# Kernel optimization log

Hardware: AMD Instinct MI355X
Metric: run time of the kernel (lower is better)

## Reference

```python
import jax, jax.numpy as jnp
import numpy as np

EPS = 1e-6
N_HEADS = 32
N_KV_HEADS = 8
HEAD_DIM = 64


def _rmsnorm(x, scale):
    xf = x.astype(jnp.float32)
    y = xf * jax.lax.rsqrt(jnp.mean(xf * xf, axis=-1, keepdims=True) + EPS)
    return y.astype(x.dtype) * scale


def _rope(t, cos, sin):
    # t: [B,S,H,D]; cos/sin: [S,D//2] -> broadcast [1,S,1,D//2]
    tr = t.reshape(*t.shape[:-1], HEAD_DIM // 2, 2)
    tre, tim = tr[..., 0], tr[..., 1]
    c = cos[None, :, None, :]
    s = sin[None, :, None, :]
    out_re = tre * c - tim * s
    out_im = tre * s + tim * c
    return jnp.stack([out_re, out_im], axis=-1).reshape(t.shape)


def setup_inputs() -> dict:
    key = jax.random.key(0)
    ks = jax.random.split(key, 8)
    B, S, D = 2, 2048, 2048
    x = jax.random.normal(ks[0], (B, S, D), dtype=jnp.float32)
    # rotary freqs: cos/sin of theta^(-2i/d) * pos, like precompute_freqs_cis
    pos = jnp.arange(S, dtype=jnp.float32)
    inv_freq = 1.0 / (10000.0 ** (jnp.arange(0, HEAD_DIM, 2, dtype=jnp.float32) / HEAD_DIM))
    angles = pos[:, None] * inv_freq[None, :]  # [S, D/2]
    freqs_cos = jnp.cos(angles)
    freqs_sin = jnp.sin(angles)
    std = 0.02
    wq = jax.random.normal(ks[1], (N_HEADS * HEAD_DIM, D), dtype=jnp.float32) * std
    wk = jax.random.normal(ks[2], (N_KV_HEADS * HEAD_DIM, D), dtype=jnp.float32) * std
    wv = jax.random.normal(ks[3], (N_KV_HEADS * HEAD_DIM, D), dtype=jnp.float32) * std
    wo = jax.random.normal(ks[4], (D, N_HEADS * HEAD_DIM), dtype=jnp.float32) * std
    q_scale = jnp.ones((HEAD_DIM,), dtype=jnp.float32)
    k_scale = jnp.ones((HEAD_DIM,), dtype=jnp.float32)
    return {"x": x, "freqs_cos": freqs_cos, "freqs_sin": freqs_sin,
            "wq": wq, "wk": wk, "wv": wv, "wo": wo,
            "q_scale": q_scale, "k_scale": k_scale}


def reference(x, freqs_cos, freqs_sin, wq, wk, wv, wo, q_scale, k_scale):
    B, S, D = x.shape
    n_rep = N_HEADS // N_KV_HEADS
    xq = (x @ wq.T).reshape(B, S, N_HEADS, HEAD_DIM)
    xk = (x @ wk.T).reshape(B, S, N_KV_HEADS, HEAD_DIM)
    xv = (x @ wv.T).reshape(B, S, N_KV_HEADS, HEAD_DIM)
    # per-head QK RMSNorm
    xq = _rmsnorm(xq, q_scale)
    xk = _rmsnorm(xk, k_scale)
    # rotary embedding
    xq = _rope(xq, freqs_cos, freqs_sin)
    xk = _rope(xk, freqs_cos, freqs_sin)
    # GQA repeat_kv
    keys = jnp.repeat(xk, n_rep, axis=2)    # [B,S,H,Dh]
    values = jnp.repeat(xv, n_rep, axis=2)
    # SDPA, causal
    q = xq.transpose(0, 2, 1, 3)  # [B,H,S,Dh]
    k = keys.transpose(0, 2, 1, 3)
    v = values.transpose(0, 2, 1, 3)
    scale = 1.0 / jnp.sqrt(jnp.float32(HEAD_DIM))
    scores = jnp.einsum('bhqd,bhkd->bhqk', q, k) * scale
    causal = jnp.tril(jnp.ones((S, S), dtype=bool))
    scores = jnp.where(causal[None, None], scores, jnp.finfo(scores.dtype).min)
    probs = jax.nn.softmax(scores, axis=-1)
    out = jnp.einsum('bhqk,bhkd->bhqd', probs, v)
    out = out.transpose(0, 2, 1, 3).reshape(B, S, N_HEADS * HEAD_DIM)
    return out @ wo.T
```

## Files before the change

kernel.cpp:

```cpp
#include <hip/hip_runtime.h>
#include <hip/hip_bf16.h>
#include <math.h>

#define S_LEN   2048
#define DMODEL  2048
#define NHEADS  32
#define NKV     8
#define HD      64
#define MTOK    4096
#define KVDIM   512

typedef short s16x8 __attribute__((ext_vector_type(8)));
typedef float f32x4 __attribute__((ext_vector_type(4)));

__device__ __forceinline__ ushort f2bf(float f) {
    union { float f; uint u; } a; a.f = f;
    return (ushort)((a.u + 0x7fffu + ((a.u >> 16) & 1u)) >> 16);
}
__device__ __forceinline__ float bf2f(ushort h) {
    union { uint u; float f; } a; a.u = ((uint)h) << 16; return a.f;
}

__global__ __launch_bounds__(256) void csplit(const float* __restrict__ src,
                                              ushort* __restrict__ dh,
                                              ushort* __restrict__ dl, int n8) {
    const int i = blockIdx.x * 256 + threadIdx.x;
    if (i >= n8) return;
    float4 a = ((const float4*)src)[2 * i];
    float4 b = ((const float4*)src)[2 * i + 1];
    float f[8] = {a.x, a.y, a.z, a.w, b.x, b.y, b.z, b.w};
    s16x8 h, l;
#pragma unroll
    for (int j = 0; j < 8; ++j) {
        ushort hb = f2bf(f[j]);
        h[j] = (short)hb;
        l[j] = (short)f2bf(f[j] - bf2f(hb));
    }
    ((s16x8*)dh)[i] = h;
    ((s16x8*)dl)[i] = l;
}

__global__ __launch_bounds__(256) void gemm_bs(const ushort* __restrict__ Ahg,
                                               const ushort* __restrict__ Alg,
                                               const ushort* __restrict__ Bhg,
                                               const ushort* __restrict__ Blg,
                                               float* __restrict__ C,
                                               int M, int N, int K) {
    __shared__ ushort Ah[128 * 32];
    __shared__ ushort Al[128 * 32];
    __shared__ ushort Bh[128 * 32];
    __shared__ ushort Bl[128 * 32];

    const int tid  = threadIdx.x;
    const int wave = tid >> 6;
    const int lane = tid & 63;
    const int wr   = (wave >> 1) * 64;
    const int wc   = (wave & 1) * 64;
    const int m0   = blockIdx.y * 128;
    const int n0   = blockIdx.x * 128;

    const int srow = tid >> 2;
    const int skq  = (tid & 3) * 8;
    const int soff = srow * 32 + skq;

    const ushort* pAh = Ahg + (size_t)(m0 + srow) * K + skq;
    const ushort* pAl = Alg + (size_t)(m0 + srow) * K + skq;
    const ushort* pBh = Bhg + (size_t)(n0 + srow) * K + skq;
    const ushort* pBl = Blg + (size_t)(n0 + srow) * K + skq;
    const size_t r64 = (size_t)64 * K;

    const int frow = lane & 15;
    const int fk   = (lane >> 4) * 8;

    f32x4 acc[4][4] = {};

    s16x8 rAh0 = *(const s16x8*)(pAh), rAh1 = *(const s16x8*)(pAh + r64);
    s16x8 rAl0 = *(const s16x8*)(pAl), rAl1 = *(const s16x8*)(pAl + r64);
    s16x8 rBh0 = *(const s16x8*)(pBh), rBh1 = *(const s16x8*)(pBh + r64);
    s16x8 rBl0 = *(const s16x8*)(pBl), rBl1 = *(const s16x8*)(pBl + r64);

    for (int k0 = 0; k0 < K; k0 += 32) {
        __syncthreads();
        *(s16x8*)(Ah + soff) = rAh0;  *(s16x8*)(Ah + soff + 64 * 32) = rAh1;
        *(s16x8*)(Al + soff) = rAl0;  *(s16x8*)(Al + soff + 64 * 32) = rAl1;
        *(s16x8*)(Bh + soff) = rBh0;  *(s16x8*)(Bh + soff + 64 * 32) = rBh1;
        *(s16x8*)(Bl + soff) = rBl0;  *(s16x8*)(Bl + soff + 64 * 32) = rBl1;

        if (k0 + 32 < K) {
            rAh0 = *(const s16x8*)(pAh + k0 + 32); rAh1 = *(const s16x8*)(pAh + r64 + k0 + 32);
            rAl0 = *(const s16x8*)(pAl + k0 + 32); rAl1 = *(const s16x8*)(pAl + r64 + k0 + 32);
            rBh0 = *(const s16x8*)(pBh + k0 + 32); rBh1 = *(const s16x8*)(pBh + r64 + k0 + 32);
            rBl0 = *(const s16x8*)(pBl + k0 + 32); rBl1 = *(const s16x8*)(pBl + r64 + k0 + 32);
        }
        __syncthreads();

        s16x8 ah[4], al[4], bh[4], bl[4];
#pragma unroll
        for (int mi = 0; mi < 4; ++mi) {
            int off = (wr + mi * 16 + frow) * 32 + fk;
            ah[mi] = *(const s16x8*)(Ah + off);
            al[mi] = *(const s16x8*)(Al + off);
        }
#pragma unroll
        for (int nj = 0; nj < 4; ++nj) {
            int off = (wc + nj * 16 + frow) * 32 + fk;
            bh[nj] = *(const s16x8*)(Bh + off);
            bl[nj] = *(const s16x8*)(Bl + off);
        }
#pragma unroll
        for (int mi = 0; mi < 4; ++mi)
#pragma unroll
            for (int nj = 0; nj < 4; ++nj) {
                acc[mi][nj] = __builtin_amdgcn_mfma_f32_16x16x32_bf16(ah[mi], bh[nj], acc[mi][nj], 0, 0, 0);
                acc[mi][nj] = __builtin_amdgcn_mfma_f32_16x16x32_bf16(ah[mi], bl[nj], acc[mi][nj], 0, 0, 0);
                acc[mi][nj] = __builtin_amdgcn_mfma_f32_16x16x32_bf16(al[mi], bh[nj], acc[mi][nj], 0, 0, 0);
            }
    }

    const int crow = (lane >> 4) * 4;
    const int ccol = lane & 15;
#pragma unroll
    for (int mi = 0; mi < 4; ++mi)
#pragma unroll
        for (int r = 0; r < 4; ++r) {
            float* cp = C + (size_t)(m0 + wr + mi * 16 + crow + r) * N + n0 + wc + ccol;
#pragma unroll
            for (int nj = 0; nj < 4; ++nj)
                cp[nj * 16] = acc[mi][nj][r];
        }
}

__global__ __launch_bounds__(256) void rmsrope_split(const float* __restrict__ src,
                                                     const float* __restrict__ scale,
                                                     const float* __restrict__ fcos,
                                                     const float* __restrict__ fsin,
                                                     int nheads, int rowstride,
                                                     ushort* __restrict__ dh,
                                                     ushort* __restrict__ dl,
                                                     float prescale) {
    const int wid   = blockIdx.x * 4 + (threadIdx.x >> 6);
    const int lane  = threadIdx.x & 63;
    const int token = wid / nheads;
    const int h     = wid - token * nheads;
    const int s     = token & (S_LEN - 1);

    const size_t idx = (size_t)token * rowstride + h * HD + lane;
    float v = src[idx];

    float ss = v * v;
#pragma unroll
    for (int off = 32; off; off >>= 1) ss += __shfl_xor(ss, off);

    float y = v * (1.0f / sqrtf(ss * (1.0f / 64.0f) + 1e-6f)) * scale[lane];

    const int j = lane >> 1;
    float c  = fcos[s * (HD / 2) + j];
    float sn = fsin[s * (HD / 2) + j];
    float partner = __shfl_xor(y, 1);
    float o = (lane & 1) ? fmaf(partner, sn, y * c)
                         : fmaf(y, c, -partner * sn);
    o *= prescale;

    ushort hb = f2bf(o);
    dh[idx] = hb;
    dl[idx] = f2bf(o - bf2f(hb));
}

__global__ __launch_bounds__(256) void vtrans(const float* __restrict__ xv,
                                              ushort* __restrict__ vh,
                                              ushort* __restrict__ vl) {
    __shared__ float T[64][65];
    const int tid = threadIdx.x;
    const int st  = blockIdx.x;
    const int bk  = blockIdx.y;
    const int b   = bk >> 3, kvh = bk & 7;

    const int r = tid >> 2, cq = (tid & 3) * 16;
    const float* src = xv + (size_t)(b * S_LEN + st * 64 + r) * KVDIM + kvh * HD + cq;
#pragma unroll
    for (int i = 0; i < 4; ++i) {
        float4 f = *(const float4*)(src + 4 * i);
        T[r][cq + 4 * i + 0] = f.x; T[r][cq + 4 * i + 1] = f.y;
        T[r][cq + 4 * i + 2] = f.z; T[r][cq + 4 * i + 3] = f.w;
    }
    __syncthreads();

    const int d = tid >> 2, sq = (tid & 3) * 16;
    s16x8 hv[2], lv[2];
#pragma unroll
    for (int half = 0; half < 2; ++half)
#pragma unroll
        for (int j = 0; j < 8; ++j) {
            float f = T[sq + half * 8 + j][d];
            ushort hb = f2bf(f);
            hv[half][j] = (short)hb;
            lv[half][j] = (short)f2bf(f - bf2f(hb));
        }
    ushort* oh = vh + (size_t)(bk * HD + d) * S_LEN + st * 64 + sq;
    ushort* ol = vl + (size_t)(bk * HD + d) * S_LEN + st * 64 + sq;
    *(s16x8*)(oh) = hv[0]; *(s16x8*)(oh + 8) = hv[1];
    *(s16x8*)(ol) = lv[0]; *(s16x8*)(ol + 8) = lv[1];
}

__global__ __launch_bounds__(256) void flash_attn(const ushort* __restrict__ qh_g,
                                                  const ushort* __restrict__ ql_g,
                                                  const ushort* __restrict__ kh_g,
                                                  const ushort* __restrict__ kl_g,
                                                  const ushort* __restrict__ vh_g,
                                                  const ushort* __restrict__ vl_g,
                                                  float* __restrict__ ao) {
    __shared__ ushort Kh[64 * 72];
    __shared__ ushort Kl[64 * 72];
    __shared__ ushort Vh[64 * 72];
    __shared__ ushort Vl[64 * 72];
    __shared__ ushort Ph[4][32 * 72];
    __shared__ ushort Pl[4][32 * 72];

    const int tid    = threadIdx.x;
    const int w      = tid >> 6;
    const int lanelo = tid & 15;
    const int g      = (tid >> 4) & 3;
    const int bh     = blockIdx.y;
    const int b      = bh >> 5;
    const int h      = bh & 31;
    const int kvh    = h >> 2;

    const int srow = tid >> 2;
    const int sh   = (tid & 3) * 16;

    const ushort* kbh = kh_g + (size_t)(b * S_LEN) * KVDIM + kvh * HD;
    const ushort* kbl = kl_g + (size_t)(b * S_LEN) * KVDIM + kvh * HD;
    const ushort* vbh = vh_g + (size_t)((b * NKV + kvh) * HD) * S_LEN;
    const ushort* vbl = vl_g + (size_t)((b * NKV + kvh) * HD) * S_LEN;

#pragma unroll 1
    for (int sub = 0; sub < 2; ++sub) {
        const int qt  = sub ? (15 - blockIdx.x) : blockIdx.x;
        const int q0  = qt * 128;
        const int nkt = 2 * qt + 2;

        s16x8 qfh[2][2], qfl[2][2];
#pragma unroll
        for (int mi = 0; mi < 2; ++mi) {
            const size_t qoff = (size_t)(b * S_LEN + q0 + 32 * w + 16 * mi + lanelo) * DMODEL
                              + h * HD + 8 * g;
            qfh[mi][0] = *(const s16x8*)(qh_g + qoff);
            qfh[mi][1] = *(const s16x8*)(qh_g + qoff + 32);
            qfl[mi][0] = *(const s16x8*)(ql_g + qoff);
            qfl[mi][1] = *(const s16x8*)(ql_g + qoff + 32);
        }

        s16x8 rkh0, rkh1, rkl0, rkl1, rvh0, rvh1, rvl0, rvl1;
        {
            const size_t ko = (size_t)srow * KVDIM + sh;
            const size_t vo = (size_t)srow * S_LEN + sh;
            rkh0 = *(const s16x8*)(kbh + ko);  rkh1 = *(const s16x8*)(kbh + ko + 8);
            rkl0 = *(const s16x8*)(kbl + ko);  rkl1 = *(const s16x8*)(kbl + ko + 8);
            rvh0 = *(const s16x8*)(vbh + vo);  rvh1 = *(const s16x8*)(vbh + vo + 8);
            rvl0 = *(const s16x8*)(vbl + vo);  rvl1 = *(const s16x8*)(vbl + vo + 8);
        }

        float m_[2][4], l_[2][4];
        f32x4 O[2][4] = {};
#pragma unroll
        for (int mi = 0; mi < 2; ++mi)
#pragma unroll
            for (int r = 0; r < 4; ++r) { m_[mi][r] = -1e30f; l_[mi][r] = 0.0f; }

        for (int kt = 0; kt < nkt; ++kt) {
            __syncthreads();
            const int lo = srow * 72 + sh;
            *(s16x8*)(Kh + lo) = rkh0;  *(s16x8*)(Kh + lo + 8) = rkh1;
            *(s16x8*)(Kl + lo) = rkl0;  *(s16x8*)(Kl + lo + 8) = rkl1;
            *(s16x8*)(Vh + lo) = rvh0;  *(s16x8*)(Vh + lo + 8) = rvh1;
            *(s16x8*)(Vl + lo) = rvl0;  *(s16x8*)(Vl + lo + 8) = rvl1;
            if (kt + 1 < nkt) {
                const size_t ko = (size_t)((kt + 1) * 64 + srow) * KVDIM + sh;
                const size_t vo = (size_t)srow * S_LEN + (kt + 1) * 64 + sh;
                rkh0 = *(const s16x8*)(kbh + ko);  rkh1 = *(const s16x8*)(kbh + ko + 8);
                rkl0 = *(const s16x8*)(kbl + ko);  rkl1 = *(const s16x8*)(kbl + ko + 8);
                rvh0 = *(const s16x8*)(vbh + vo);  rvh1 = *(const s16x8*)(vbh + vo + 8);
                rvl0 = *(const s16x8*)(vbl + vo);  rvl1 = *(const s16x8*)(vbl + vo + 8);
            }
            __syncthreads();

            f32x4 sc[2][4] = {};
#pragma unroll
            for (int n = 0; n < 4; ++n) {
                const int off = (16 * n + lanelo) * 72 + 8 * g;
                s16x8 kh0 = *(const s16x8*)(Kh + off), kh1 = *(const s16x8*)(Kh + off + 32);
                s16x8 kl0 = *(const s16x8*)(Kl + off), kl1 = *(const s16x8*)(Kl + off + 32);
#pragma unroll
                for (int mi = 0; mi < 2; ++mi) {
                    sc[mi][n] = __builtin_amdgcn_mfma_f32_16x16x32_bf16(qfh[mi][0], kh0, sc[mi][n], 0, 0, 0);
                    sc[mi][n] = __builtin_amdgcn_mfma_f32_16x16x32_bf16(qfh[mi][1], kh1, sc[mi][n], 0, 0, 0);
                    sc[mi][n] = __builtin_amdgcn_mfma_f32_16x16x32_bf16(qfh[mi][0], kl0, sc[mi][n], 0, 0, 0);
                    sc[mi][n] = __builtin_amdgcn_mfma_f32_16x16x32_bf16(qfh[mi][1], kl1, sc[mi][n], 0, 0, 0);
                    sc[mi][n] = __builtin_amdgcn_mfma_f32_16x16x32_bf16(qfl[mi][0], kh0, sc[mi][n], 0, 0, 0);
                    sc[mi][n] = __builtin_amdgcn_mfma_f32_16x16x32_bf16(qfl[mi][1], kh1, sc[mi][n], 0, 0, 0);
                }
            }

            if (kt >= 2 * qt) {
#pragma unroll
                for (int mi = 0; mi < 2; ++mi)
#pragma unroll
                    for (int n = 0; n < 4; ++n) {
                        const int key = kt * 64 + 16 * n + lanelo;
                        const int qrow = q0 + 32 * w + 16 * mi + 4 * g;
#pragma unroll
                        for (int r = 0; r < 4; ++r)
                            if (key > qrow + r) sc[mi][n][r] = -1e30f;
                    }
            }

#pragma unroll
            for (int mi = 0; mi < 2; ++mi)
#pragma unroll
                for (int r = 0; r < 4; ++r) {
                    float mx = fmaxf(fmaxf(sc[mi][0][r], sc[mi][1][r]),
                                     fmaxf(sc[mi][2][r], sc[mi][3][r]));
#pragma unroll
                    for (int off = 1; off < 16; off <<= 1) mx = fmaxf(mx, __shfl_xor(mx, off));
                    float mnew = fmaxf(m_[mi][r], mx);
                    float corr = __expf(m_[mi][r] - mnew);
                    float ps = 0.f;
#pragma unroll
                    for (int n = 0; n < 4; ++n) {
                        float p = __expf(sc[mi][n][r] - mnew);
                        ushort phb = f2bf(p);
                        const int po = (16 * mi + 4 * g + r) * 72 + 16 * n + lanelo;
                        Ph[w][po] = phb;
                        Pl[w][po] = f2bf(p - bf2f(phb));
                        ps += p;
                    }
#pragma unroll
                    for (int off = 1; off < 16; off <<= 1) ps += __shfl_xor(ps, off);
                    l_[mi][r] = l_[mi][r] * corr + ps;
                    m_[mi][r] = mnew;
#pragma unroll
                    for (int n = 0; n < 4; ++n) O[mi][n][r] *= corr;
                }

            s16x8 pf[2][4];
#pragma unroll
            for (int mi = 0; mi < 2; ++mi) {
                const int po = (16 * mi + lanelo) * 72 + 8 * g;
                pf[mi][0] = *(const s16x8*)(Ph[w] + po);
                pf[mi][1] = *(const s16x8*)(Ph[w] + po + 32);
                pf[mi][2] = *(const s16x8*)(Pl[w] + po);
                pf[mi][3] = *(const s16x8*)(Pl[w] + po + 32);
            }
#pragma unroll
            for (int n = 0; n < 4; ++n) {
                const int vo = (16 * n + lanelo) * 72 + 8 * g;
                s16x8 vh0 = *(const s16x8*)(Vh + vo), vh1 = *(const s16x8*)(Vh + vo + 32);
                s16x8 vl0 = *(const s16x8*)(Vl + vo), vl1 = *(const s16x8*)(Vl + vo + 32);
#pragma unroll
                for (int mi = 0; mi < 2; ++mi) {
                    O[mi][n] = __builtin_amdgcn_mfma_f32_16x16x32_bf16(pf[mi][0], vh0, O[mi][n], 0, 0, 0);
                    O[mi][n] = __builtin_amdgcn_mfma_f32_16x16x32_bf16(pf[mi][1], vh1, O[mi][n], 0, 0, 0);
                    O[mi][n] = __builtin_amdgcn_mfma_f32_16x16x32_bf16(pf[mi][0], vl0, O[mi][n], 0, 0, 0);
                    O[mi][n] = __builtin_amdgcn_mfma_f32_16x16x32_bf16(pf[mi][1], vl1, O[mi][n], 0, 0, 0);
                    O[mi][n] = __builtin_amdgcn_mfma_f32_16x16x32_bf16(pf[mi][2], vh0, O[mi][n], 0, 0, 0);
                    O[mi][n] = __builtin_amdgcn_mfma_f32_16x16x32_bf16(pf[mi][3], vh1, O[mi][n], 0, 0, 0);
                }
            }
        }

#pragma unroll
        for (int mi = 0; mi < 2; ++mi)
#pragma unroll
            for (int n = 0; n < 4; ++n)
#pragma unroll
                for (int r = 0; r < 4; ++r) {
                    const int q = q0 + 32 * w + 16 * mi + 4 * g + r;
                    ao[(size_t)(b * S_LEN + q) * DMODEL + h * HD + 16 * n + lanelo] =
                        O[mi][n][r] / l_[mi][r];
                }
    }
}

extern "C" void kernel_launch(void* const* d_in, const int* in_sizes, int n_in,
                              void* d_out, int out_size, void* d_ws, size_t ws_size,
                              hipStream_t stream) {
    const float* x  = (const float*)d_in[0];
    const float* fc = (const float*)d_in[1];
    const float* fs = (const float*)d_in[2];
    const float* wq = (const float*)d_in[3];
    const float* wk = (const float*)d_in[4];
    const float* wv = (const float*)d_in[5];
    const float* wo = (const float*)d_in[6];
    const float* qs = (const float*)d_in[7];
    const float* ks = (const float*)d_in[8];
    float* out = (float*)d_out;

    char* p = (char*)d_ws;
    auto take = [&](size_t bytes) { char* r = p; p += bytes; return r; };
    ushort* wqh = (ushort*)take(8388608);   ushort* wql = (ushort*)take(8388608);
    ushort* wkh = (ushort*)take(2097152);   ushort* wkl = (ushort*)take(2097152);
    ushort* wvh = (ushort*)take(2097152);   ushort* wvl = (ushort*)take(2097152);
    ushort* woh = (ushort*)take(8388608);   ushort* wol = (ushort*)take(8388608);
    ushort* xh  = (ushort*)take(16777216);  ushort* xl  = (ushort*)take(16777216);
    float*  xq32 = (float*)take(33554432);
    float*  xk32 = (float*)take(8388608);
    float*  xv32 = (float*)take(8388608);
    ushort* qh  = (ushort*)take(16777216);  ushort* ql  = (ushort*)take(16777216);
    ushort* kh  = (ushort*)take(4194304);   ushort* kl  = (ushort*)take(4194304);
    ushort* vth = (ushort*)take(4194304);   ushort* vtl = (ushort*)take(4194304);
    ushort* aoh = xh;
    ushort* aol = xl;
    float*  ao32 = xq32;

    csplit<<<4096, 256, 0, stream>>>(x,  xh,  xl,  1048576);
    csplit<<<2048, 256, 0, stream>>>(wq, wqh, wql, 524288);
    csplit<<<512,  256, 0, stream>>>(wk, wkh, wkl, 131072);
    csplit<<<512,  256, 0, stream>>>(wv, wvh, wvl, 131072);
    csplit<<<2048, 256, 0, stream>>>(wo, woh, wol, 524288);

    gemm_bs<<<dim3(16, 32), 256, 0, stream>>>(xh, xl, wqh, wql, xq32, MTOK, DMODEL, DMODEL);
    gemm_bs<<<dim3(4,  32), 256, 0, stream>>>(xh, xl, wkh, wkl, xk32, MTOK, KVDIM,  DMODEL);
    gemm_bs<<<dim3(4,  32), 256, 0, stream>>>(xh, xl, wvh, wvl, xv32, MTOK, KVDIM,  DMODEL);

    rmsrope_split<<<MTOK * NHEADS / 4, 256, 0, stream>>>(xq32, qs, fc, fs, NHEADS, DMODEL, qh, ql, 0.125f);
    rmsrope_split<<<MTOK * NKV / 4,    256, 0, stream>>>(xk32, ks, fc, fs, NKV,    KVDIM,  kh, kl, 1.0f);
    vtrans<<<dim3(32, 16), 256, 0, stream>>>(xv32, vth, vtl);

    flash_attn<<<dim3(8, 64), 256, 0, stream>>>(qh, ql, kh, kl, vth, vtl, ao32);

    csplit<<<4096, 256, 0, stream>>>(ao32, aoh, aol, 1048576);
    gemm_bs<<<dim3(16, 32), 256, 0, stream>>>(aoh, aol, woh, wol, out, MTOK, DMODEL, DMODEL);
}
```

Baseline: 694.4 us.

## Use direct global-to-LDS loads, merge K/V GEMMs, fuse output split into attention

The GEMM stops staging tiles through registers and uses global_load_lds to copy 16-byte chunks straight into shared memory. This drops the register prefetch, so loads are no longer overlapped with compute across iterations. The K and V weight matrices are concatenated so a single GEMM produces both projections. The attention kernel now writes the bf16 hi/lo split of its output directly, removing one fp32 round trip and a separate split kernel, and the P split is simplified to truncation instead of rounding.

```diff
diff --git a/kernel.cpp b/kernel.cpp
--- a/kernel.cpp
+++ b/kernel.cpp
@@ -19,6 +19,12 @@
 }
 __device__ __forceinline__ float bf2f(ushort h) {
     union { uint u; float f; } a; a.u = ((uint)h) << 16; return a.f;
+}
+
+__device__ __forceinline__ void gload16(const void* g, void* l) {
+    __builtin_amdgcn_global_load_lds(
+        (const __attribute__((address_space(1))) void*)g,
+        (__attribute__((address_space(3))) void*)l, 16, 0, 0);
 }
 
 __global__ __launch_bounds__(256) void csplit(const float* __restrict__ src,
@@ -61,7 +67,6 @@
 
     const int srow = tid >> 2;
     const int skq  = (tid & 3) * 8;
-    const int soff = srow * 32 + skq;
 
     const ushort* pAh = Ahg + (size_t)(m0 + srow) * K + skq;
     const ushort* pAl = Alg + (size_t)(m0 + srow) * K + skq;
@@ -69,29 +74,22 @@
     const ushort* pBl = Blg + (size_t)(n0 + srow) * K + skq;
     const size_t r64 = (size_t)64 * K;
 
+    ushort* const lA0  = Ah + wave * 512;  ushort* const lA1  = Ah + 64 * 32 + wave * 512;
+    ushort* const lAl0 = Al + wave * 512;  ushort* const lAl1 = Al + 64 * 32 + wave * 512;
+    ushort* const lB0  = Bh + wave * 512;  ushort* const lB1  = Bh + 64 * 32 + wave * 512;
+    ushort* const lBl0 = Bl + wave * 512;  ushort* const lBl1 = Bl + 64 * 32 + wave * 512;
+
     const int frow = lane & 15;
     const int fk   = (lane >> 4) * 8;
 
     f32x4 acc[4][4] = {};
 
-    s16x8 rAh0 = *(const s16x8*)(pAh), rAh1 = *(const s16x8*)(pAh + r64);
-    s16x8 rAl0 = *(const s16x8*)(pAl), rAl1 = *(const s16x8*)(pAl + r64);
-    s16x8 rBh0 = *(const s16x8*)(pBh), rBh1 = *(const s16x8*)(pBh + r64);
-    s16x8 rBl0 = *(const s16x8*)(pBl), rBl1 = *(const s16x8*)(pBl + r64);
-
     for (int k0 = 0; k0 < K; k0 += 32) {
         __syncthreads();
-        *(s16x8*)(Ah + soff) = rAh0;  *(s16x8*)(Ah + soff + 64 * 32) = rAh1;
-        *(s16x8*)(Al + soff) = rAl0;  *(s16x8*)(Al + soff + 64 * 32) = rAl1;
-        *(s16x8*)(Bh + soff) = rBh0;  *(s16x8*)(Bh + soff + 64 * 32) = rBh1;
-        *(s16x8*)(Bl + soff) = rBl0;  *(s16x8*)(Bl + soff + 64 * 32) = rBl1;
-
-        if (k0 + 32 < K) {
-            rAh0 = *(const s16x8*)(pAh + k0 + 32); rAh1 = *(const s16x8*)(pAh + r64 + k0 + 32);
-            rAl0 = *(const s16x8*)(pAl + k0 + 32); rAl1 = *(const s16x8*)(pAl + r64 + k0 + 32);
-            rBh0 = *(const s16x8*)(pBh + k0 + 32); rBh1 = *(const s16x8*)(pBh + r64 + k0 + 32);
-            rBl0 = *(const s16x8*)(pBl + k0 + 32); rBl1 = *(const s16x8*)(pBl + r64 + k0 + 32);
-        }
+        gload16(pAh + k0, lA0);        gload16(pAh + r64 + k0, lA1);
+        gload16(pAl + k0, lAl0);       gload16(pAl + r64 + k0, lAl1);
+        gload16(pBh + k0, lB0);        gload16(pBh + r64 + k0, lB1);
+        gload16(pBl + k0, lBl0);       gload16(pBl + r64 + k0, lBl1);
         __syncthreads();
 
         s16x8 ah[4], al[4], bh[4], bl[4];
@@ -134,7 +132,7 @@
                                                      const float* __restrict__ scale,
                                                      const float* __restrict__ fcos,
                                                      const float* __restrict__ fsin,
-                                                     int nheads, int rowstride,
+                                                     int nheads, int instride, int outstride,
                                                      ushort* __restrict__ dh,
                                                      ushort* __restrict__ dl,
                                                      float prescale) {
@@ -144,8 +142,7 @@
     const int h     = wid - token * nheads;
     const int s     = token & (S_LEN - 1);
 
-    const size_t idx = (size_t)token * rowstride + h * HD + lane;
-    float v = src[idx];
+    float v = src[(size_t)token * instride + h * HD + lane];
 
     float ss = v * v;
 #pragma unroll
@@ -161,12 +158,14 @@
                          : fmaf(y, c, -partner * sn);
     o *= prescale;
 
+    const size_t oidx = (size_t)token * outstride + h * HD + lane;
     ushort hb = f2bf(o);
-    dh[idx] = hb;
-    dl[idx] = f2bf(o - bf2f(hb));
+    dh[oidx] = hb;
+    dl[oidx] = f2bf(o - bf2f(hb));
 }
 
 __global__ __launch_bounds__(256) void vtrans(const float* __restrict__ xv,
+                                              int instride,
                                               ushort* __restrict__ vh,
                                               ushort* __restrict__ vl) {
     __shared__ float T[64][65];
@@ -176,7 +175,7 @@
     const int b   = bk >> 3, kvh = bk & 7;
 
     const int r = tid >> 2, cq = (tid & 3) * 16;
-    const float* src = xv + (size_t)(b * S_LEN + st * 64 + r) * KVDIM + kvh * HD + cq;
+    const float* src = xv + (size_t)(b * S_LEN + st * 64 + r) * instride + kvh * HD + cq;
 #pragma unroll
     for (int i = 0; i < 4; ++i) {
         float4 f = *(const float4*)(src + 4 * i);
@@ -208,7 +207,8 @@
                                                   const ushort* __restrict__ kl_g,
                                                   const ushort* __restrict__ vh_g,
                                                   const ushort* __restrict__ vl_g,
-                                                  float* __restrict__ ao) {
+                                                  ushort* __restrict__ aoh,
+                                                  ushort* __restrict__ aol) {
     __shared__ ushort Kh[64 * 72];
     __shared__ ushort Kl[64 * 72];
     __shared__ ushort Vh[64 * 72];
@@ -232,6 +232,9 @@
     const ushort* kbl = kl_g + (size_t)(b * S_LEN) * KVDIM + kvh * HD;
     const ushort* vbh = vh_g + (size_t)((b * NKV + kvh) * HD) * S_LEN;
     const ushort* vbl = vl_g + (size_t)((b * NKV + kvh) * HD) * S_LEN;
+
+    ushort* const Phw = Ph[w];
+    ushort* const Plw = Pl[w];
 
 #pragma unroll 1
     for (int sub = 0; sub < 2; ++sub) {
@@ -328,10 +331,11 @@
 #pragma unroll
                     for (int n = 0; n < 4; ++n) {
                         float p = __expf(sc[mi][n][r] - mnew);
-                        ushort phb = f2bf(p);
+                        uint pu = __float_as_uint(p);
+                        float plo = p - __uint_as_float(pu & 0xffff0000u);
                         const int po = (16 * mi + 4 * g + r) * 72 + 16 * n + lanelo;
-                        Ph[w][po] = phb;
-                        Pl[w][po] = f2bf(p - bf2f(phb));
+                        Phw[po] = (ushort)(pu >> 16);
+                        Plw[po] = (ushort)(__float_as_uint(plo) >> 16);
                         ps += p;
                     }
 #pragma unroll
@@ -346,10 +350,10 @@
 #pragma unroll
             for (int mi = 0; mi < 2; ++mi) {
                 const int po = (16 * mi + lanelo) * 72 + 8 * g;
-                pf[mi][0] = *(const s16x8*)(Ph[w] + po);
-                pf[mi][1] = *(const s16x8*)(Ph[w] + po + 32);
-                pf[mi][2] = *(const s16x8*)(Pl[w] + po);
-                pf[mi][3] = *(const s16x8*)(Pl[w] + po + 32);
+                pf[mi][0] = *(const s16x8*)(Phw + po);
+                pf[mi][1] = *(const s16x8*)(Phw + po + 32);
+                pf[mi][2] = *(const s16x8*)(Plw + po);
+                pf[mi][3] = *(const s16x8*)(Plw + po + 32);
             }
 #pragma unroll
             for (int n = 0; n < 4; ++n) {
@@ -375,8 +379,11 @@
 #pragma unroll
                 for (int r = 0; r < 4; ++r) {
                     const int q = q0 + 32 * w + 16 * mi + 4 * g + r;
-                    ao[(size_t)(b * S_LEN + q) * DMODEL + h * HD + 16 * n + lanelo] =
-                        O[mi][n][r] / l_[mi][r];
+                    const size_t o = (size_t)(b * S_LEN + q) * DMODEL + h * HD + 16 * n + lanelo;
+                    float v = O[mi][n][r] / l_[mi][r];
+                    ushort hb = f2bf(v);
+                    aoh[o] = hb;
+                    aol[o] = f2bf(v - bf2f(hb));
                 }
     }
 }
@@ -397,37 +404,32 @@
 
     char* p = (char*)d_ws;
     auto take = [&](size_t bytes) { char* r = p; p += bytes; return r; };
-    ushort* wqh = (ushort*)take(8388608);   ushort* wql = (ushort*)take(8388608);
-    ushort* wkh = (ushort*)take(2097152);   ushort* wkl = (ushort*)take(2097152);
-    ushort* wvh = (ushort*)take(2097152);   ushort* wvl = (ushort*)take(2097152);
-    ushort* woh = (ushort*)take(8388608);   ushort* wol = (ushort*)take(8388608);
-    ushort* xh  = (ushort*)take(16777216);  ushort* xl  = (ushort*)take(16777216);
-    float*  xq32 = (float*)take(33554432);
-    float*  xk32 = (float*)take(8388608);
-    float*  xv32 = (float*)take(8388608);
-    ushort* qh  = (ushort*)take(16777216);  ushort* ql  = (ushort*)take(16777216);
-    ushort* kh  = (ushort*)take(4194304);   ushort* kl  = (ushort*)take(4194304);
-    ushort* vth = (ushort*)take(4194304);   ushort* vtl = (ushort*)take(4194304);
+    ushort* wqh  = (ushort*)take(8388608);   ushort* wql  = (ushort*)take(8388608);
+    ushort* wkvh = (ushort*)take(4194304);   ushort* wkvl = (ushort*)take(4194304);
+    ushort* woh  = (ushort*)take(8388608);   ushort* wol  = (ushort*)take(8388608);
+    ushort* xh   = (ushort*)take(16777216);  ushort* xl   = (ushort*)take(16777216);
+    float*  xq32  = (float*)take(33554432);
+    float*  xkv32 = (float*)take(16777216);
+    ushort* qh   = (ushort*)take(16777216);  ushort* ql   = (ushort*)take(16777216);
+    ushort* kh   = (ushort*)take(4194304);   ushort* kl   = (ushort*)take(4194304);
+    ushort* vth  = (ushort*)take(4194304);   ushort* vtl  = (ushort*)take(4194304);
     ushort* aoh = xh;
     ushort* aol = xl;
-    float*  ao32 = xq32;
 
     csplit<<<4096, 256, 0, stream>>>(x,  xh,  xl,  1048576);
     csplit<<<2048, 256, 0, stream>>>(wq, wqh, wql, 524288);
-    csplit<<<512,  256, 0, stream>>>(wk, wkh, wkl, 131072);
-    csplit<<<512,  256, 0, stream>>>(wv, wvh, wvl, 131072);
+    csplit<<<512,  256, 0, stream>>>(wk, wkvh,                wkvl,                131072);
+    csplit<<<512,  256, 0, stream>>>(wv, wkvh + 512 * DMODEL, wkvl + 512 * DMODEL, 131072);
     csplit<<<2048, 256, 0, stream>>>(wo, woh, wol, 524288);
 
-    gemm_bs<<<dim3(16, 32), 256, 0, stream>>>(xh, xl, wqh, wql, xq32, MTOK, DMODEL, DMODEL);
-    gemm_bs<<<dim3(4,  32), 256, 0, stream>>>(xh, xl, wkh, wkl, xk32, MTOK, KVDIM,  DMODEL);
-    gemm_bs<<<dim3(4,  32), 256, 0, stream>>>(xh, xl, wvh, wvl, xv32, MTOK, KVDIM,  DMODEL);
-
-    rmsrope_split<<<MTOK * NHEADS / 4, 256, 0, stream>>>(xq32, qs, fc, fs, NHEADS, DMODEL, qh, ql, 0.125f);
-    rmsrope_split<<<MTOK * NKV / 4,    256, 0, stream>>>(xk32, ks, fc, fs, NKV,    KVDIM,  kh, kl, 1.0f);
-    vtrans<<<dim3(32, 16), 256, 0, stream>>>(xv32, vth, vtl);
-
-    flash_attn<<<dim3(8, 64), 256, 0, stream>>>(qh, ql, kh, kl, vth, vtl, ao32);
-
-    csplit<<<4096, 256, 0, stream>>>(ao32, aoh, aol, 1048576);
+    gemm_bs<<<dim3(16, 32), 256, 0, stream>>>(xh, xl, wqh,  wql,  xq32,  MTOK, DMODEL, DMODEL);
+    gemm_bs<<<dim3(8,  32), 256, 0, stream>>>(xh, xl, wkvh, wkvl, xkv32, MTOK, 1024,   DMODEL);
+
+    rmsrope_split<<<MTOK * NHEADS / 4, 256, 0, stream>>>(xq32, qs, fc, fs, NHEADS, DMODEL, DMODEL, qh, ql, 0.125f);
+    rmsrope_split<<<MTOK * NKV / 4,    256, 0, stream>>>(xkv32, ks, fc, fs, NKV,   1024,   KVDIM,  kh, kl, 1.0f);
+    vtrans<<<dim3(32, 16), 256, 0, stream>>>(xkv32 + 512, 1024, vth, vtl);
+
+    flash_attn<<<dim3(8, 64), 256, 0, stream>>>(qh, ql, kh, kl, vth, vtl, aoh, aol);
+
     gemm_bs<<<dim3(16, 32), 256, 0, stream>>>(aoh, aol, woh, wol, out, MTOK, DMODEL, DMODEL);
 }
```

Measured after the change: 649.5 us. -6.5%, faster.
